# Kernel tuning notes

Measured on AMD Instinct MI355X. Metric: run time of the kernel, lower is better.

Reference implementation:

```python
import jax, jax.numpy as jnp
import numpy as np
from jax import lax

B, N, D_FEAT = 16, 4096, 20
NPOINT, NSAMPLE = 1024, 32
MLP = [64, 64, 128]
IN_CH = 3 + 1 + D_FEAT  # grouped_xyz_norm(3) + L2 norm(1) + grouped_depth_norm(20)
BN_EPS = 1e-5


def setup_inputs() -> dict:
    key = jax.random.key(0)
    ks = jax.random.split(key, 20)
    inp = {
        "xyz": jax.random.normal(ks[0], (B, 3, N), dtype=jnp.float32),
        "feature": jax.random.normal(ks[1], (B, N, D_FEAT), dtype=jnp.float32),
    }
    last = IN_CH
    kidx = 2
    for li, out_ch in enumerate(MLP):
        inp[f"w{li}"] = jax.random.normal(ks[kidx], (out_ch, last), dtype=jnp.float32) * (1.0 / np.sqrt(last)); kidx += 1
        inp[f"b{li}"] = jax.random.normal(ks[kidx], (out_ch,), dtype=jnp.float32) * 0.01; kidx += 1
        inp[f"g{li}"] = 1.0 + 0.1 * jax.random.normal(ks[kidx], (out_ch,), dtype=jnp.float32); kidx += 1
        inp[f"bt{li}"] = 0.1 * jax.random.normal(ks[kidx], (out_ch,), dtype=jnp.float32); kidx += 1
        last = out_ch
    return inp


def square_distance(src, dst):
    # [B,S,C] x [B,M,C] -> [B,S,M]
    d = -2.0 * jnp.einsum("bsc,bmc->bsm", src, dst)
    d = d + jnp.sum(src * src, -1)[:, :, None]
    d = d + jnp.sum(dst * dst, -1)[:, None, :]
    return d


def farthest_point_sample(pts, npoint):
    # pts: [B,N,C]; deterministic start at index 0 (torch uses random start)
    b, n, _ = pts.shape
    bidx = jnp.arange(b)

    def step(carry, _):
        dist, far = carry
        centroid = pts[bidx, far]                      # [B,C]
        d = jnp.sum((pts - centroid[:, None, :]) ** 2, -1)  # [B,N]
        dist = jnp.minimum(dist, d)
        nxt = jnp.argmax(dist, -1)
        return (dist, nxt), far

    init = (jnp.full((b, n), 1e10, pts.dtype), jnp.zeros((b,), jnp.int32))
    _, idx = lax.scan(step, init, None, length=npoint)
    return idx.T  # [B,npoint]


def _gather_groups(points, idx):
    # points [B,N,C], idx [B,S,K] -> [B,S,K,C]
    return jax.vmap(lambda p, i: p[i])(points, idx)


def conv_bn_relu(x, w, b, g, bt):
    # x [B,C,K,S]; 1x1 conv = channel matmul; BN in training mode (batch stats, biased var)
    y = jnp.einsum("bcks,oc->boks", x, w) + b[None, :, None, None]
    mu = jnp.mean(y, axis=(0, 2, 3), keepdims=True)
    var = jnp.mean((y - mu) ** 2, axis=(0, 2, 3), keepdims=True)
    y = (y - mu) * lax.rsqrt(var + BN_EPS)
    y = y * g[None, :, None, None] + bt[None, :, None, None]
    return jax.nn.relu(y)


def reference(xyz, feature, w0, b0, g0, bt0, w1, b1, g1, bt1, w2, b2, g2, bt2):
    xyz_n = jnp.transpose(xyz, (0, 2, 1))              # [B,N,3]
    combined = jnp.concatenate([xyz_n, feature], -1)   # [B,N,23]
    fps_idx = farthest_point_sample(combined, NPOINT)  # [B,S]

    new_bin = jnp.take_along_axis(feature, fps_idx[:, :, None], axis=1)  # [B,S,20]
    new_xyz = jnp.take_along_axis(xyz_n, fps_idx[:, :, None], axis=1)    # [B,S,3]

    sqd = square_distance(new_bin, feature) + square_distance(new_xyz, xyz_n)  # [B,S,N]
    idx = jnp.argsort(sqd, axis=-1)[:, :, :NSAMPLE]    # [B,S,K]

    gxyz = _gather_groups(xyz_n, idx)                  # [B,S,K,3]
    gfeat = _gather_groups(feature, idx)               # [B,S,K,20]
    gxyz_norm = gxyz - new_xyz[:, :, None, :]
    gdep_norm = gfeat - new_bin[:, :, None, :]
    nrm = jnp.sqrt(jnp.maximum(jnp.sum(gxyz_norm ** 2, -1, keepdims=True), 1e-12))
    new_points = jnp.concatenate([gxyz_norm, nrm, gdep_norm], -1)  # [B,S,K,24]

    x = jnp.transpose(new_points, (0, 3, 2, 1))        # [B,24,K,S]
    for (w, b, g, bt) in [(w0, b0, g0, bt0), (w1, b1, g1, bt1), (w2, b2, g2, bt2)]:
        x = conv_bn_relu(x, w, b, g, bt)
    out = jnp.max(x, axis=2)                           # [B,128,S]
    return jnp.transpose(new_xyz, (0, 2, 1)), out, new_bin
```

## Files before the change

kernel.cpp:

```cpp
#include <hip/hip_runtime.h>

#define BB 16
#define NN 4096
#define DFEAT 20
#define SS 1024
#define KK 32
#define MM (BB*SS*KK)

#define WS_STATS   0ull
#define WS_PARAMS  8192ull
#define WS_FPSIDX  12288ull
#define WS_CENT    81920ull
#define WS_KNN     1654784ull
#define WS_COMB    3751936ull
#define WS_YB      10043392ull
#define WS_NEED    77152256ull

typedef float v2f __attribute__((ext_vector_type(2)));

static __device__ __forceinline__ unsigned short f2bf(float f){
    unsigned u = __float_as_uint(f);
    unsigned r = (u + 0x7FFFu + ((u >> 16) & 1u)) >> 16;
    return (unsigned short)r;
}
static __device__ __forceinline__ float bf2f(unsigned short v){
    return __uint_as_float((unsigned)v << 16);
}
static __device__ __forceinline__ void pinv2(v2f& x){
    asm volatile("" : "+v"(x));
}

static __device__ __forceinline__ unsigned long long max64(unsigned long long a, unsigned long long b){
    return a > b ? a : b;
}
template<int CTRL>
static __device__ __forceinline__ unsigned long long dpp_move64(unsigned long long k){
    int tlo = __builtin_amdgcn_update_dpp(0, (int)(unsigned)k,         CTRL, 0xf, 0xf, true);
    int thi = __builtin_amdgcn_update_dpp(0, (int)(unsigned)(k >> 32), CTRL, 0xf, 0xf, true);
    return ((unsigned long long)(unsigned)thi << 32) | (unsigned)tlo;
}

__global__ void k_zstats(double* __restrict__ stats){
    int t = threadIdx.x;
#pragma unroll
    for (int i = 0; i < 4; ++i) stats[i*256 + t] = 0.0;
}

__global__ void k_fail(float* __restrict__ out, int n){
    int i = blockIdx.x * 256 + threadIdx.x;
    if (i < n) out[i] = 0.f;
}

__global__ __launch_bounds__(256) void k_build(const float* __restrict__ xyz,
                                               const float* __restrict__ feat,
                                               float* __restrict__ comb)
{
    int idx = blockIdx.x * 256 + threadIdx.x;
    int b = idx >> 12, j = idx & 4095;
    float c[24];
    c[0] = xyz[((size_t)b*3 + 0)*NN + j];
    c[1] = xyz[((size_t)b*3 + 1)*NN + j];
    c[2] = xyz[((size_t)b*3 + 2)*NN + j];
    const float* f = feat + ((size_t)b*NN + j)*DFEAT;
#pragma unroll
    for (int d = 0; d < 20; ++d) c[3+d] = f[d];
    c[23] = 0.f;
    float* out = comb + (size_t)idx * 24;
#pragma unroll
    for (int q = 0; q < 6; ++q)
        ((float4*)out)[q] = make_float4(c[4*q], c[4*q+1], c[4*q+2], c[4*q+3]);
}

__global__ __launch_bounds__(512)
__attribute__((amdgpu_waves_per_eu(2, 2)))
void k_fps(const float* __restrict__ comb,
           int* __restrict__ fpsidx)
{
    int b = blockIdx.x, t = threadIdx.x;
    const float* C = comb + (size_t)b * NN * 24;
    v2f pt2[4][24];
    float dist[8];
#pragma unroll
    for (int p = 0; p < 8; ++p){
        const float4* r = (const float4*)(C + (size_t)(t + 512*p) * 24);
#pragma unroll
        for (int q = 0; q < 6; ++q){
            float4 v = r[q];
            pt2[p>>1][4*q+0][p&1] = v.x;
            pt2[p>>1][4*q+1][p&1] = v.y;
            pt2[p>>1][4*q+2][p&1] = v.z;
            pt2[p>>1][4*q+3][p&1] = v.w;
        }
        dist[p] = 1e10f;
    }
#pragma unroll
    for (int k = 0; k < 4; ++k)
#pragma unroll
        for (int q = 0; q < 23; ++q) pinv2(pt2[k][q]);

    __shared__ __align__(16) unsigned long long wkey[2][8];
    __shared__ __align__(16) float wpt[2][8][24];
    int lane = t & 63, w = t >> 6;
    unsigned nt = 0xFFFFFFFFu - (unsigned)t;
    int far = 0;

    float cc[24];
    {
        const float4* crow = (const float4*)C;
#pragma unroll
        for (int q = 0; q < 6; ++q){
            float4 cv = crow[q];
            cc[4*q] = cv.x; cc[4*q+1] = cv.y; cc[4*q+2] = cv.z; cc[4*q+3] = cv.w;
        }
    }

    for (int s = 0; s < SS; ++s){
        if (t == 0) fpsidx[b*SS + s] = far;
        v2f acc2[4];
#pragma unroll
        for (int k = 0; k < 4; ++k){
            v2f d0 = pt2[k][0] - cc[0];
            acc2[k] = d0 * d0;
        }
#pragma unroll
        for (int q = 1; q < 23; ++q){
            float cq = cc[q];
#pragma unroll
            for (int k = 0; k < 4; ++k){
                v2f dd = pt2[k][q] - cq;
                acc2[k] = __builtin_elementwise_fma(dd, dd, acc2[k]);
            }
        }
        unsigned maxbits = 0u;
#pragma unroll
        for (int p = 0; p < 8; ++p){
            dist[p] = fminf(dist[p], acc2[p>>1][p&1]);
            unsigned bb2 = __float_as_uint(dist[p]);
            maxbits = bb2 > maxbits ? bb2 : maxbits;
        }
        int pstar = 0;
#pragma unroll
        for (int p = 7; p >= 0; --p)
            if (__float_as_uint(dist[p]) == maxbits) pstar = p;
        unsigned long long key = ((unsigned long long)maxbits << 32)
                               | (unsigned long long)(nt - ((unsigned)pstar << 9));

        key = max64(key, dpp_move64<0x111>(key));
        key = max64(key, dpp_move64<0x112>(key));
        key = max64(key, dpp_move64<0x114>(key));
        key = max64(key, dpp_move64<0x118>(key));
        key = max64(key, dpp_move64<0x142>(key));
        key = max64(key, dpp_move64<0x143>(key));
        unsigned long long wk;
        {
            int slo = __builtin_amdgcn_readlane((int)(unsigned)key, 63);
            int shi = __builtin_amdgcn_readlane((int)(unsigned)(key >> 32), 63);
            wk = ((unsigned long long)(unsigned)shi << 32) | (unsigned)slo;
        }
        int par = s & 1;
        if (lane == 0) wkey[par][w] = wk;
        unsigned widx = 0xFFFFFFFFu - (unsigned)(wk & 0xFFFFFFFFull);
        if (t == (int)(widx & 511u)){
            int pw = (int)(widx >> 9);
            float* dst = wpt[par][w];
            switch (pw){
#define PE(P,q) pt2[(P)>>1][q][(P)&1]
#define STASH(P) case P: \
                ((float4*)dst)[0] = make_float4(PE(P,0),PE(P,1),PE(P,2),PE(P,3)); \
                ((float4*)dst)[1] = make_float4(PE(P,4),PE(P,5),PE(P,6),PE(P,7)); \
                ((float4*)dst)[2] = make_float4(PE(P,8),PE(P,9),PE(P,10),PE(P,11)); \
                ((float4*)dst)[3] = make_float4(PE(P,12),PE(P,13),PE(P,14),PE(P,15)); \
                ((float4*)dst)[4] = make_float4(PE(P,16),PE(P,17),PE(P,18),PE(P,19)); \
                ((float4*)dst)[5] = make_float4(PE(P,20),PE(P,21),PE(P,22),0.f); \
                break;
            STASH(0) STASH(1) STASH(2) STASH(3)
            STASH(4) STASH(5) STASH(6) STASH(7)
#undef STASH
#undef PE
            }
        }
        __syncthreads();
        unsigned long long k2 = wkey[par][lane & 7];
        k2 = max64(k2, dpp_move64<0x121>(k2));
        k2 = max64(k2, dpp_move64<0x122>(k2));
        k2 = max64(k2, dpp_move64<0x124>(k2));
        far = (int)(0xFFFFFFFFu - (unsigned)(k2 & 0xFFFFFFFFull));
        int wg = (far & 511) >> 6;
        const float4* crow = (const float4*)wpt[par][wg];
#pragma unroll
        for (int q = 0; q < 6; ++q){
            float4 cv = crow[q];
            cc[4*q] = cv.x; cc[4*q+1] = cv.y; cc[4*q+2] = cv.z; cc[4*q+3] = cv.w;
        }
    }
}

__global__ __launch_bounds__(256) void k_gather(const float* __restrict__ comb,
                                                const int* __restrict__ fpsidx,
                                                float* __restrict__ cent,
                                                float* __restrict__ out0,
                                                float* __restrict__ out2)
{
    int idx = blockIdx.x * 256 + threadIdx.x;
    int b = idx >> 10, s = idx & 1023;
    int j = fpsidx[idx];
    const float* row = comb + ((size_t)b*NN + j) * 24;
    float* cr = cent + (size_t)idx * 24;
#pragma unroll
    for (int q = 0; q < 6; ++q) ((float4*)cr)[q] = ((const float4*)row)[q];
#pragma unroll
    for (int c = 0; c < 3; ++c) out0[((size_t)b*3 + c)*SS + s] = row[c];
    float* o2 = out2 + (size_t)idx * 20;
#pragma unroll
    for (int d = 0; d < 20; ++d) o2[d] = row[3 + d];
}

__global__ __launch_bounds__(256) void k_knn(const float* __restrict__ comb,
                                             const float* __restrict__ cent,
                                             int* __restrict__ knn)
{
    int w = threadIdx.x >> 6, lane = threadIdx.x & 63;
    int r = blockIdx.x * 4 + w;
    int b = r >> 10;
    const float* crow = cent + (size_t)r * 24;
    const float* P0 = comb + (size_t)b * NN * 24;
    double cc[24];
#pragma unroll
    for (int q = 0; q < 24; ++q) cc[q] = (double)crow[q];
    unsigned u[64];
#pragma unroll
    for (int k = 0; k < 64; ++k){
        int j = k*64 + lane;
        const float4* pr = (const float4*)(P0 + (size_t)j * 24);
        double acc = 0.0;
#pragma unroll
        for (int q = 0; q < 6; ++q){
            float4 v = pr[q];
            double d0 = (double)v.x - cc[4*q];
            double d1 = (double)v.y - cc[4*q+1];
            double d2 = (double)v.z - cc[4*q+2];
            double d3 = (double)v.w - cc[4*q+3];
            acc += d0*d0; acc += d1*d1; acc += d2*d2; acc += d3*d3;
        }
        u[k] = __float_as_uint((float)acc);
    }
    unsigned lo = 0u, hi = 0xFFFFFFFFu;
    for (int it = 0; it < 32; ++it){
        unsigned mid = lo + ((hi - lo) >> 1);
        int cnt = 0;
#pragma unroll
        for (int k = 0; k < 64; ++k) cnt += (u[k] <= mid) ? 1 : 0;
#pragma unroll
        for (int off = 32; off > 0; off >>= 1) cnt += __shfl_xor(cnt, off);
        if (cnt >= KK) hi = mid; else lo = mid + 1;
    }
    unsigned T = lo;
    int* orow = knn + (size_t)r * KK;
    unsigned long long lmask = (1ull << lane) - 1ull;
    int pos = 0;
#pragma unroll
    for (int k = 0; k < 64; ++k){
        bool lt = (u[k] < T);
        unsigned long long mk = __ballot(lt);
        if (lt) orow[pos + __popcll(mk & lmask)] = k*64 + lane;
        pos += __popcll(mk);
    }
#pragma unroll
    for (int k = 0; k < 64; ++k){
        if (pos >= KK) break;
        bool eq = (u[k] == T);
        unsigned long long mk = __ballot(eq);
        int rk = __popcll(mk & lmask);
        if (eq && (pos + rk) < KK) orow[pos + rk] = k*64 + lane;
        pos += __popcll(mk);
    }
}

__global__ __launch_bounds__(256) void k_l1(const float* __restrict__ comb,
                                            const float* __restrict__ cent,
                                            const int* __restrict__ knn,
                                            const float* __restrict__ w0,
                                            const float* __restrict__ b0,
                                            unsigned short* __restrict__ yb)
{
    __shared__ float Wt[24][64];
    __shared__ float Xt[24][68];
    int t = threadIdx.x;
    int m_base = blockIdx.x * 64;
    for (int i = t; i < 1536; i += 256){
        int o = i / 24, c = i - o*24;
        Wt[c][o] = w0[i];
    }
    {
        int sm = t & 63, g = t >> 6;
        int m = m_base + sm;
        int b = m >> 15;
        int row = m >> 5;
        int j = knn[m];
        const float* P  = comb + ((size_t)b*NN + j) * 24;
        const float* Cc = cent + (size_t)row * 24;
        if (g == 0){
            float dx = P[0]-Cc[0], dy = P[1]-Cc[1], dz = P[2]-Cc[2];
            Xt[0][sm] = dx; Xt[1][sm] = dy; Xt[2][sm] = dz;
            float n2 = dx*dx; n2 = fmaf(dy, dy, n2); n2 = fmaf(dz, dz, n2);
            Xt[3][sm] = sqrtf(fmaxf(n2, 1e-12f));
            Xt[4][sm] = P[3] - Cc[3];
            Xt[5][sm] = P[4] - Cc[4];
        } else {
#pragma unroll
            for (int cq = 0; cq < 6; ++cq){
                int c = 6*g + cq;
                Xt[c][sm] = P[c-1] - Cc[c-1];
            }
        }
    }
    __syncthreads();
    int i = t >> 4, jj = t & 15;
    float acc[4][4] = {};
#pragma unroll
    for (int c = 0; c < 24; ++c){
        float4 wv = *(const float4*)&Wt[c][i*4];
        float4 xv = *(const float4*)&Xt[c][jj*4];
        float wr[4] = {wv.x, wv.y, wv.z, wv.w};
        float xr[4] = {xv.x, xv.y, xv.z, xv.w};
#pragma unroll
        for (int a = 0; a < 4; ++a)
#pragma unroll
            for (int q = 0; q < 4; ++q) acc[a][q] = fmaf(wr[a], xr[q], acc[a][q]);
    }
#pragma unroll
    for (int oi = 0; oi < 4; ++oi){
        int o = i*4 + oi;
        float bb = b0[o];
        ushort4 rv;
        rv.x = f2bf(acc[oi][0]+bb); rv.y = f2bf(acc[oi][1]+bb);
        rv.z = f2bf(acc[oi][2]+bb); rv.w = f2bf(acc[oi][3]+bb);
        *(ushort4*)&yb[(size_t)o*MM + m_base + jj*4] = rv;
    }
}

__global__ __launch_bounds__(256) void k_stats(const unsigned short* __restrict__ y,
                                               double* __restrict__ stats)
{
    const int chunks = 8;
    int c = blockIdx.x / chunks, ch = blockIdx.x % chunks;
    size_t base = (size_t)c * MM + (size_t)ch * (MM / chunks);
    double s1 = 0.0, s2 = 0.0;
    const unsigned short* p = y + base;
    for (int i = threadIdx.x; i < MM/chunks; i += 256){
        float v = bf2f(p[i]);
        s1 += v; s2 += (double)v * v;
    }
#pragma unroll
    for (int off = 32; off > 0; off >>= 1){
        s1 += __shfl_xor(s1, off);
        s2 += __shfl_xor(s2, off);
    }
    __shared__ double ps1[4], ps2[4];
    int w = threadIdx.x >> 6, lane = threadIdx.x & 63;
    if (lane == 0){ ps1[w] = s1; ps2[w] = s2; }
    __syncthreads();
    if (threadIdx.x == 0){
        atomicAdd(&stats[c*2 + 0], ps1[0]+ps1[1]+ps1[2]+ps1[3]);
        atomicAdd(&stats[c*2 + 1], ps2[0]+ps2[1]+ps2[2]+ps2[3]);
    }
}

__global__ void k_affine(const double* __restrict__ stats, float* __restrict__ params, int C)
{
    int c = threadIdx.x;
    if (c < C){
        double mu = stats[c*2] / (double)MM;
        double var = stats[c*2 + 1] / (double)MM - mu*mu;
        params[c*2 + 0] = (float)mu;
        params[c*2 + 1] = (float)(1.0 / sqrt(var + 1e-5));
    }
}

__global__ __launch_bounds__(256) void k_l2(unsigned short* __restrict__ yb,
                                            const float* __restrict__ prm,
                                            const float* __restrict__ gg,
                                            const float* __restrict__ bt,
                                            const float* __restrict__ w,
                                            const float* __restrict__ bias)
{
    __shared__ float Wt[64][64];
    __shared__ float Xt[64][68];
    int t = threadIdx.x;
    int m_base = blockIdx.x * 64;
    for (int i = t; i < 4096; i += 256){
        int o = i >> 6, c = i & 63;
        Wt[c][o] = w[i];
    }
#pragma unroll
    for (int rp = 0; rp < 16; ++rp){
        int idx = rp*256 + t;
        int c = idx >> 6, mm2 = idx & 63;
        float v = bf2f(yb[(size_t)c*MM + m_base + mm2]);
        float t1 = (v - prm[c*2]) * prm[c*2 + 1];
        Xt[c][mm2] = fmaxf(fmaf(t1, gg[c], bt[c]), 0.f);
    }
    __syncthreads();
    int i = t >> 4, jj = t & 15;
    float acc[4][4] = {};
#pragma unroll
    for (int c = 0; c < 64; ++c){
        float4 wv = *(const float4*)&Wt[c][i*4];
        float4 xv = *(const float4*)&Xt[c][jj*4];
        float wr[4] = {wv.x, wv.y, wv.z, wv.w};
        float xr[4] = {xv.x, xv.y, xv.z, xv.w};
#pragma unroll
        for (int a = 0; a < 4; ++a)
#pragma unroll
            for (int q = 0; q < 4; ++q) acc[a][q] = fmaf(wr[a], xr[q], acc[a][q]);
    }
#pragma unroll
    for (int oi = 0; oi < 4; ++oi){
        int o = i*4 + oi;
        float bb = bias[o];
        ushort4 rv;
        rv.x = f2bf(acc[oi][0]+bb); rv.y = f2bf(acc[oi][1]+bb);
        rv.z = f2bf(acc[oi][2]+bb); rv.w = f2bf(acc[oi][3]+bb);
        *(ushort4*)&yb[(size_t)o*MM + m_base + jj*4] = rv;
    }
}

__global__ __launch_bounds__(256) void k_l3s(const unsigned short* __restrict__ yb,
                                             const float* __restrict__ prm,
                                             const float* __restrict__ gg,
                                             const float* __restrict__ bt,
                                             const float* __restrict__ w,
                                             const float* __restrict__ bias,
                                             double* __restrict__ stats)
{
    __shared__ float Wt[64][128];
    __shared__ float Xt[64][68];
    int t = threadIdx.x;
    for (int i = t; i < 8192; i += 256){
        int o = i >> 6, c = i & 63;
        Wt[c][o] = w[i];
    }
    int i = t >> 4, jj = t & 15;
    double s1[8] = {}, s2[8] = {};
    for (int tt = 0; tt < 16; ++tt){
        int m_base = (blockIdx.x * 16 + tt) * 64;
        __syncthreads();
#pragma unroll
        for (int rp = 0; rp < 16; ++rp){
            int idx = rp*256 + t;
            int c = idx >> 6, mm2 = idx & 63;
            float v = bf2f(yb[(size_t)c*MM + m_base + mm2]);
            float t1 = (v - prm[c*2]) * prm[c*2 + 1];
            Xt[c][mm2] = fmaxf(fmaf(t1, gg[c], bt[c]), 0.f);
        }
        __syncthreads();
        float acc[8][4] = {};
#pragma unroll
        for (int c = 0; c < 64; ++c){
            float4 w0v = *(const float4*)&Wt[c][i*8];
            float4 w1v = *(const float4*)&Wt[c][i*8 + 4];
            float4 xv  = *(const float4*)&Xt[c][jj*4];
            float wr[8] = {w0v.x, w0v.y, w0v.z, w0v.w, w1v.x, w1v.y, w1v.z, w1v.w};
            float xr[4] = {xv.x, xv.y, xv.z, xv.w};
#pragma unroll
            for (int a = 0; a < 8; ++a)
#pragma unroll
                for (int q = 0; q < 4; ++q) acc[a][q] = fmaf(wr[a], xr[q], acc[a][q]);
        }
#pragma unroll
        for (int oi = 0; oi < 8; ++oi){
            float bb = bias[i*8 + oi];
#pragma unroll
            for (int q = 0; q < 4; ++q){
                float v = acc[oi][q] + bb;
                s1[oi] += v;
                s2[oi] += (double)v * v;
            }
        }
    }
#pragma unroll
    for (int oi = 0; oi < 8; ++oi){
#pragma unroll
        for (int off = 1; off < 16; off <<= 1){
            s1[oi] += __shfl_xor(s1[oi], off);
            s2[oi] += __shfl_xor(s2[oi], off);
        }
    }
    if (jj == 0){
#pragma unroll
        for (int oi = 0; oi < 8; ++oi){
            int o = i*8 + oi;
            atomicAdd(&stats[o*2 + 0], s1[oi]);
            atomicAdd(&stats[o*2 + 1], s2[oi]);
        }
    }
}

__global__ __launch_bounds__(256) void k_final(const unsigned short* __restrict__ yb,
                                               const float* __restrict__ prm2,
                                               const float* __restrict__ g1c,
                                               const float* __restrict__ bt1c,
                                               const float* __restrict__ w,
                                               const float* __restrict__ bias,
                                               const float* __restrict__ prm3,
                                               const float* __restrict__ g2c,
                                               const float* __restrict__ bt2c,
                                               float* __restrict__ out1)
{
    __shared__ float Wt[64][128];
    __shared__ float Xt[64][68];
    int t = threadIdx.x;
    int m_base = blockIdx.x * 64;
    for (int i = t; i < 8192; i += 256){
        int o = i >> 6, c = i & 63;
        Wt[c][o] = w[i];
    }
#pragma unroll
    for (int rp = 0; rp < 16; ++rp){
        int idx = rp*256 + t;
        int c = idx >> 6, mm2 = idx & 63;
        float v = bf2f(yb[(size_t)c*MM + m_base + mm2]);
        float t1 = (v - prm2[c*2]) * prm2[c*2 + 1];
        Xt[c][mm2] = fmaxf(fmaf(t1, g1c[c], bt1c[c]), 0.f);
    }
    __syncthreads();
    int i = t >> 4, jj = t & 15;
    float acc[8][4] = {};
#pragma unroll
    for (int c = 0; c < 64; ++c){
        float4 w0v = *(const float4*)&Wt[c][i*8];
        float4 w1v = *(const float4*)&Wt[c][i*8 + 4];
        float4 xv  = *(const float4*)&Xt[c][jj*4];
        float wr[8] = {w0v.x, w0v.y, w0v.z, w0v.w, w1v.x, w1v.y, w1v.z, w1v.w};
        float xr[4] = {xv.x, xv.y, xv.z, xv.w};
#pragma unroll
        for (int a = 0; a < 8; ++a)
#pragma unroll
            for (int q = 0; q < 4; ++q) acc[a][q] = fmaf(wr[a], xr[q], acc[a][q]);
    }
    float mx[8];
#pragma unroll
    for (int oi = 0; oi < 8; ++oi){
        int o = i*8 + oi;
        float bb = bias[o];
        float mu = prm3[o*2], inv = prm3[o*2 + 1], gv = g2c[o], bv = bt2c[o];
        float m = 0.f;
#pragma unroll
        for (int q = 0; q < 4; ++q){
            float v = acc[oi][q] + bb;
            float r = fmaxf(fmaf((v - mu) * inv, gv, bv), 0.f);
            m = fmaxf(m, r);
        }
        mx[oi] = m;
    }
#pragma unroll
    for (int oi = 0; oi < 8; ++oi){
#pragma unroll
        for (int off = 1; off < 8; off <<= 1)
            mx[oi] = fmaxf(mx[oi], __shfl_xor(mx[oi], off));
    }
    if ((jj & 7) == 0){
        int rg = (m_base >> 5) + (jj >> 3);
        int b = rg >> 10, s = rg & 1023;
#pragma unroll
        for (int oi = 0; oi < 8; ++oi)
            out1[(size_t)b*131072 + (size_t)(i*8 + oi)*1024 + s] = mx[oi];
    }
}

extern "C" void kernel_launch(void* const* d_in, const int* in_sizes, int n_in,
                              void* d_out, int out_size, void* d_ws, size_t ws_size,
                              hipStream_t stream)
{
    const float* xyz  = (const float*)d_in[0];
    const float* feat = (const float*)d_in[1];
    const float* w0 = (const float*)d_in[2];  const float* b0  = (const float*)d_in[3];
    const float* g0 = (const float*)d_in[4];  const float* bt0 = (const float*)d_in[5];
    const float* w1 = (const float*)d_in[6];  const float* b1  = (const float*)d_in[7];
    const float* g1 = (const float*)d_in[8];  const float* bt1 = (const float*)d_in[9];
    const float* w2 = (const float*)d_in[10]; const float* b2  = (const float*)d_in[11];
    const float* g2 = (const float*)d_in[12]; const float* bt2 = (const float*)d_in[13];

    float* out0 = (float*)d_out;
    float* out1 = (float*)d_out + 49152;
    float* out2 = (float*)d_out + 49152 + 2097152;

    if (ws_size < WS_NEED){
        k_fail<<<(out_size + 255)/256, 256, 0, stream>>>((float*)d_out, out_size);
        return;
    }

    char* ws = (char*)d_ws;
    double* stats = (double*)(ws + WS_STATS);
    float* params = (float*)(ws + WS_PARAMS);
    int*   fpsidx = (int*)(ws + WS_FPSIDX);
    float* cent   = (float*)(ws + WS_CENT);
    int*   knn    = (int*)(ws + WS_KNN);
    float* comb   = (float*)(ws + WS_COMB);
    unsigned short* yb = (unsigned short*)(ws + WS_YB);

    k_zstats<<<1,    256, 0, stream>>>(stats);
    k_build <<<256,  256, 0, stream>>>(xyz, feat, comb);
    k_fps   <<<16,   512, 0, stream>>>(comb, fpsidx);
    k_gather<<<64,   256, 0, stream>>>(comb, fpsidx, cent, out0, out2);
    k_knn   <<<4096, 256, 0, stream>>>(comb, cent, knn);
    k_l1    <<<8192, 256, 0, stream>>>(comb, cent, knn, w0, b0, yb);
    k_stats <<<512,  256, 0, stream>>>(yb, stats);
    k_affine<<<1,    128, 0, stream>>>(stats, params, 64);
    k_l2    <<<8192, 256, 0, stream>>>(yb, params, g0, bt0, w1, b1);
    k_stats <<<512,  256, 0, stream>>>(yb, stats + 256);
    k_affine<<<1,    128, 0, stream>>>(stats + 256, params + 256, 64);
    k_l3s   <<<512,  256, 0, stream>>>(yb, params + 256, g1, bt1, w2, b2, stats + 512);
    k_affine<<<1,    128, 0, stream>>>(stats + 512, params + 512, 128);
    k_final <<<8192, 256, 0, stream>>>(yb, params + 256, g1, bt1, w2, b2,
                                       params + 512, g2, bt2, out1);
}
```

Before: 3.176 ms.

## Streamline FPS argmax reduction with 32-bit DPP and LDS atomic max

Rewrites the per-iteration argmax in the farthest-point-sampling kernel. The 64-bit key wave reduction becomes two 32-bit DPP max passes: first the max distance, then the index among lanes holding that max. The cross-wave combine becomes an LDS atomicMax on a rotating slot, replacing the second DPP reduction after the barrier. It also keeps distances as packed v2f min/max, buffers the selected indices in LDS and writes them to global memory once at the end. The aim is a shorter serial critical path in the 1024-step loop, at the cost of an extra readlane pass and LDS atomic contention.

```diff
diff --git a/kernel.cpp b/kernel.cpp
--- a/kernel.cpp
+++ b/kernel.cpp
@@ -30,14 +30,21 @@
     asm volatile("" : "+v"(x));
 }
 
-static __device__ __forceinline__ unsigned long long max64(unsigned long long a, unsigned long long b){
+template<int CTRL>
+static __device__ __forceinline__ unsigned dpp32_or0(unsigned x){
+    return (unsigned)__builtin_amdgcn_update_dpp(0, (int)x, CTRL, 0xf, 0xf, true);
+}
+static __device__ __forceinline__ unsigned umax32(unsigned a, unsigned b){
     return a > b ? a : b;
 }
-template<int CTRL>
-static __device__ __forceinline__ unsigned long long dpp_move64(unsigned long long k){
-    int tlo = __builtin_amdgcn_update_dpp(0, (int)(unsigned)k,         CTRL, 0xf, 0xf, true);
-    int thi = __builtin_amdgcn_update_dpp(0, (int)(unsigned)(k >> 32), CTRL, 0xf, 0xf, true);
-    return ((unsigned long long)(unsigned)thi << 32) | (unsigned)tlo;
+static __device__ __forceinline__ unsigned wave_max_u32(unsigned x){
+    x = umax32(x, dpp32_or0<0x111>(x));
+    x = umax32(x, dpp32_or0<0x112>(x));
+    x = umax32(x, dpp32_or0<0x114>(x));
+    x = umax32(x, dpp32_or0<0x118>(x));
+    x = umax32(x, dpp32_or0<0x142>(x));
+    x = umax32(x, dpp32_or0<0x143>(x));
+    return x;
 }
 
 __global__ void k_zstats(double* __restrict__ stats){
@@ -71,15 +78,13 @@
         ((float4*)out)[q] = make_float4(c[4*q], c[4*q+1], c[4*q+2], c[4*q+3]);
 }
 
-__global__ __launch_bounds__(512)
-__attribute__((amdgpu_waves_per_eu(2, 2)))
-void k_fps(const float* __restrict__ comb,
-           int* __restrict__ fpsidx)
+__global__ __launch_bounds__(512, 2) void k_fps(const float* __restrict__ comb,
+                                                int* __restrict__ fpsidx)
 {
     int b = blockIdx.x, t = threadIdx.x;
     const float* C = comb + (size_t)b * NN * 24;
     v2f pt2[4][24];
-    float dist[8];
+    v2f dist2[4];
 #pragma unroll
     for (int p = 0; p < 8; ++p){
         const float4* r = (const float4*)(C + (size_t)(t + 512*p) * 24);
@@ -91,19 +96,23 @@
             pt2[p>>1][4*q+2][p&1] = v.z;
             pt2[p>>1][4*q+3][p&1] = v.w;
         }
-        dist[p] = 1e10f;
-    }
-#pragma unroll
-    for (int k = 0; k < 4; ++k)
+    }
+#pragma unroll
+    for (int k = 0; k < 4; ++k){
+        dist2[k] = (v2f){1e10f, 1e10f};
 #pragma unroll
         for (int q = 0; q < 23; ++q) pinv2(pt2[k][q]);
-
-    __shared__ __align__(16) unsigned long long wkey[2][8];
+    }
+
     __shared__ __align__(16) float wpt[2][8][24];
+    __shared__ unsigned long long gkey[4];
+    __shared__ int fps_lds[SS];
     int lane = t & 63, w = t >> 6;
     unsigned nt = 0xFFFFFFFFu - (unsigned)t;
     int far = 0;
 
+    if (t < 4) gkey[t] = 0ull;
+
     float cc[24];
     {
         const float4* crow = (const float4*)C;
@@ -113,9 +122,10 @@
             cc[4*q] = cv.x; cc[4*q+1] = cv.y; cc[4*q+2] = cv.z; cc[4*q+3] = cv.w;
         }
     }
+    __syncthreads();
 
     for (int s = 0; s < SS; ++s){
-        if (t == 0) fpsidx[b*SS + s] = far;
+        if (t == 0) fps_lds[s] = far;
         v2f acc2[4];
 #pragma unroll
         for (int k = 0; k < 4; ++k){
@@ -131,35 +141,25 @@
                 acc2[k] = __builtin_elementwise_fma(dd, dd, acc2[k]);
             }
         }
-        unsigned maxbits = 0u;
-#pragma unroll
-        for (int p = 0; p < 8; ++p){
-            dist[p] = fminf(dist[p], acc2[p>>1][p&1]);
-            unsigned bb2 = __float_as_uint(dist[p]);
-            maxbits = bb2 > maxbits ? bb2 : maxbits;
-        }
+#pragma unroll
+        for (int k = 0; k < 4; ++k)
+            dist2[k] = __builtin_elementwise_min(dist2[k], acc2[k]);
+        v2f m01 = __builtin_elementwise_max(dist2[0], dist2[1]);
+        v2f m23 = __builtin_elementwise_max(dist2[2], dist2[3]);
+        v2f mt  = __builtin_elementwise_max(m01, m23);
+        float mf = fmaxf(mt[0], mt[1]);
+        unsigned maxbits = __float_as_uint(mf);
         int pstar = 0;
 #pragma unroll
         for (int p = 7; p >= 0; --p)
-            if (__float_as_uint(dist[p]) == maxbits) pstar = p;
-        unsigned long long key = ((unsigned long long)maxbits << 32)
-                               | (unsigned long long)(nt - ((unsigned)pstar << 9));
-
-        key = max64(key, dpp_move64<0x111>(key));
-        key = max64(key, dpp_move64<0x112>(key));
-        key = max64(key, dpp_move64<0x114>(key));
-        key = max64(key, dpp_move64<0x118>(key));
-        key = max64(key, dpp_move64<0x142>(key));
-        key = max64(key, dpp_move64<0x143>(key));
-        unsigned long long wk;
-        {
-            int slo = __builtin_amdgcn_readlane((int)(unsigned)key, 63);
-            int shi = __builtin_amdgcn_readlane((int)(unsigned)(key >> 32), 63);
-            wk = ((unsigned long long)(unsigned)shi << 32) | (unsigned)slo;
-        }
+            if (__float_as_uint(dist2[p>>1][p&1]) == maxbits) pstar = p;
+
+        unsigned M = __builtin_amdgcn_readlane((int)wave_max_u32(maxbits), 63);
+        unsigned cidx = (maxbits == M) ? (nt - ((unsigned)pstar << 9)) : 0u;
+        unsigned widxc = __builtin_amdgcn_readlane((int)wave_max_u32(cidx), 63);
+        unsigned widx  = 0xFFFFFFFFu - widxc;
+
         int par = s & 1;
-        if (lane == 0) wkey[par][w] = wk;
-        unsigned widx = 0xFFFFFFFFu - (unsigned)(wk & 0xFFFFFFFFull);
         if (t == (int)(widx & 511u)){
             int pw = (int)(widx >> 9);
             float* dst = wpt[par][w];
@@ -179,11 +179,14 @@
 #undef PE
             }
         }
+        if (lane == 63){
+            unsigned long long key = ((unsigned long long)M << 32)
+                                   | (unsigned long long)widxc;
+            atomicMax(&gkey[s & 3], key);
+        }
         __syncthreads();
-        unsigned long long k2 = wkey[par][lane & 7];
-        k2 = max64(k2, dpp_move64<0x121>(k2));
-        k2 = max64(k2, dpp_move64<0x122>(k2));
-        k2 = max64(k2, dpp_move64<0x124>(k2));
+        unsigned long long k2 = gkey[s & 3];
+        if (t == 0) gkey[(s + 2) & 3] = 0ull;
         far = (int)(0xFFFFFFFFu - (unsigned)(k2 & 0xFFFFFFFFull));
         int wg = (far & 511) >> 6;
         const float4* crow = (const float4*)wpt[par][wg];
@@ -193,6 +196,9 @@
             cc[4*q] = cv.x; cc[4*q+1] = cv.y; cc[4*q+2] = cv.z; cc[4*q+3] = cv.w;
         }
     }
+    __syncthreads();
+    fpsidx[b*SS + t]        = fps_lds[t];
+    fpsidx[b*SS + 512 + t]  = fps_lds[512 + t];
 }
 
 __global__ __launch_bounds__(256) void k_gather(const float* __restrict__ comb,
```

Measured after the change: 3.312 ms. 1.04x slower.
